# Kernel tuning notes

Hardware: AMD Instinct MI355X
Metric: run time of the kernel (lower is better)

## Reference

```python
import jax, jax.numpy as jnp
import numpy as np

B, L, ENC, DEC, ATT = 64, 1024, 1024, 1024, 1024


def setup_inputs() -> dict:
    key = jax.random.key(0)
    ks = jax.random.split(key, 8)
    s1 = 1.0 / np.sqrt(ENC)
    s2 = 1.0 / np.sqrt(DEC)
    s3 = 1.0 / np.sqrt(ATT)
    return {
        "features": jax.random.normal(ks[0], (B, L, ENC), jnp.float32),
        "hidden_state": jax.random.normal(ks[1], (B, DEC), jnp.float32),
        "W1_w": jax.random.uniform(ks[2], (ENC, ATT), jnp.float32, -s1, s1),
        "W1_b": jax.random.uniform(ks[3], (ATT,), jnp.float32, -s1, s1),
        "W2_w": jax.random.uniform(ks[4], (DEC, ATT), jnp.float32, -s2, s2),
        "W2_b": jax.random.uniform(ks[5], (ATT,), jnp.float32, -s2, s2),
        "V_w": jax.random.uniform(ks[6], (ATT,), jnp.float32, -s3, s3),
        "V_b": jax.random.uniform(ks[7], (), jnp.float32, -s3, s3),
    }


def reference(features, hidden_state, W1_w, W1_b, W2_w, W2_b, V_w, V_b):
    # proj_f: [B, L, ATT]; proj_h: [B, 1, ATT]
    proj_f = jnp.einsum('ble,ea->bla', features, W1_w) + W1_b
    proj_h = (hidden_state @ W2_w + W2_b)[:, None, :]
    scores = jnp.tanh(proj_f + proj_h) @ V_w + V_b  # [B, L]
    alpha = jax.nn.softmax(scores, axis=1)
    context = jnp.einsum('bl,ble->be', alpha, features)
    return alpha, context
```

## Files before the change

### kernel.cpp

```cpp
#include <hip/hip_runtime.h>
#include <hip/hip_bf16.h>


typedef __bf16 bf16x8 __attribute__((ext_vector_type(8)));
typedef float floatx4 __attribute__((ext_vector_type(4)));
typedef unsigned short ushort_t;
typedef unsigned long long u64;

__device__ __forceinline__ ushort_t f2b(float x) {
    union { float f; unsigned u; } v; v.f = x;
    unsigned r = (v.u + 0x7fffu + ((v.u >> 16) & 1u)) >> 16;
    return (ushort_t)r;
}

__device__ __forceinline__ float b2f(ushort_t u) {
    union { unsigned u; float f; } v; v.u = (unsigned)u << 16; return v.f;
}

__device__ __forceinline__ u64 pack4(float4 f) {
    return (u64)f2b(f.x) | ((u64)f2b(f.y) << 16) |
           ((u64)f2b(f.z) << 32) | ((u64)f2b(f.w) << 48);
}

__device__ __forceinline__ void gload_lds16(const void* g, void* l) {
    __builtin_amdgcn_global_load_lds(
        (const __attribute__((address_space(1))) void*)g,
        (__attribute__((address_space(3))) void*)l, 16, 0, 0);
}

__device__ __forceinline__ float fast_tanh(float x) {
    const float ax = fabsf(x);
    const float t  = __expf(-2.0f * ax);
    const float r  = (1.0f - t) * __builtin_amdgcn_rcpf(1.0f + t);
    return copysignf(r, x);
}

__global__ __launch_bounds__(256) void convert_feat_kernel(
    const float* __restrict__ feat, ushort_t* __restrict__ featb) {
    const size_t idx = ((size_t)blockIdx.x * 256 + threadIdx.x) * 8;
    const float4 f0 = *(const float4*)(feat + idx);
    const float4 f1 = *(const float4*)(feat + idx + 4);
    *(u64*)(featb + idx)     = pack4(f0);
    *(u64*)(featb + idx + 4) = pack4(f1);
}

__global__ __launch_bounds__(256) void transpose_w1_kernel(
    const float* __restrict__ w1, ushort_t* __restrict__ w1t) {
    __shared__ ushort_t tile[64][65];
    const int k0 = blockIdx.x * 64, n0 = blockIdx.y * 64;
    const int tr = threadIdx.x >> 6;
    const int tc = threadIdx.x & 63;
#pragma unroll
    for (int i = 0; i < 16; i++) {
        int r = i * 4 + tr;
        tile[tc][r] = f2b(w1[(size_t)(k0 + r) * 1024 + n0 + tc]);
    }
    __syncthreads();
#pragma unroll
    for (int i = 0; i < 16; i++) {
        int r = i * 4 + tr;
        w1t[(size_t)(n0 + r) * 1024 + k0 + tc] = tile[r][tc];
    }
}

__global__ __launch_bounds__(256) void projh_kernel(
    const float* __restrict__ hidden, const float* __restrict__ w2,
    const float* __restrict__ w2b, const float* __restrict__ w1b,
    float* __restrict__ ph) {
    const int b  = blockIdx.y;
    const int al = threadIdx.x & 63;
    const int eg = threadIdx.x >> 6;
    const int a  = blockIdx.x * 64 + al;
    const float* h = hidden + b * 1024;
    float sum = 0.f;
    const int e0 = eg * 256;
#pragma unroll 8
    for (int e = e0; e < e0 + 256; e++)
        sum += h[e] * w2[(size_t)e * 1024 + a];
    __shared__ float red[256];
    red[threadIdx.x] = sum;
    __syncthreads();
    if (threadIdx.x < 64)
        ph[b * 1024 + a] = w2b[a] + w1b[a] + red[al] + red[al + 64] +
                           red[al + 128] + red[al + 192];
}

#define LOG2E2 2.885390082f

__global__ __launch_bounds__(256) void gemm_scores_bf16_kernel(
    const ushort_t* __restrict__ featb,
    const ushort_t* __restrict__ w1t,
    const float* __restrict__ ph,
    const float* __restrict__ vw,
    float* __restrict__ part) {
    __shared__ ushort_t As[128 * 64];
    __shared__ ushort_t Bs[128 * 64];
    __shared__ float cbias[128];
    __shared__ float vvw[128];

    const int tid = threadIdx.x;
    const int lid = blockIdx.y * 8 + blockIdx.x;
    const int c   = lid & 7;
    const int rr  = lid >> 3;
    const int mt  = (rr >> 3) * 8 + c;
    const int nt  = rr & 7;
    const int n0 = nt * 128;
    const int m0 = mt * 128;
    const int b  = m0 >> 10;

    if (tid < 128) {
        cbias[tid] = ph[(b << 10) + n0 + tid];
        vvw[tid]   = vw[n0 + tid];
    }

    const int wave = tid >> 6;
    const int lane = tid & 63;
    const int wr = (wave >> 1) * 64;
    const int wc = (wave & 1) * 64;
    const int q  = lane >> 4;
    const int l15 = lane & 15;

    floatx4 acc[4][4] = {};

    const int srow = lane >> 3;
    const int scol = ((lane & 7) ^ srow) << 3;

    const ushort_t* aBase = featb + (size_t)m0 * 1024;
    const ushort_t* bBase = w1t  + (size_t)n0 * 1024;

    int aoff[4][2], boff[4][2];
#pragma unroll
    for (int t = 0; t < 4; t++) {
        const int ra = wr + t * 16 + l15;
        const int rb = wc + t * 16 + l15;
        aoff[t][0] = ra * 64 + (((q    ) ^ (ra & 7)) << 3);
        aoff[t][1] = ra * 64 + (((q + 4) ^ (ra & 7)) << 3);
        boff[t][0] = rb * 64 + (((q    ) ^ (rb & 7)) << 3);
        boff[t][1] = rb * 64 + (((q + 4) ^ (rb & 7)) << 3);
    }

    for (int kt = 0; kt < 1024; kt += 64) {
#pragma unroll
        for (int p = 0; p < 4; p++) {
            const int seg = wave * 4 + p;
            const int row = seg * 8 + srow;
            gload_lds16(aBase + (size_t)row * 1024 + kt + scol, As + seg * 512);
            gload_lds16(bBase + (size_t)row * 1024 + kt + scol, Bs + seg * 512);
        }
        __syncthreads();
#pragma unroll
        for (int h = 0; h < 2; h++) {
            bf16x8 af[4], bfr[4];
#pragma unroll
            for (int t = 0; t < 4; t++) af[t]  = *(const bf16x8*)&As[aoff[t][h]];
#pragma unroll
            for (int t = 0; t < 4; t++) bfr[t] = *(const bf16x8*)&Bs[boff[t][h]];
#pragma unroll
            for (int tm = 0; tm < 4; tm++)
#pragma unroll
                for (int tn = 0; tn < 4; tn++)
                    acc[tm][tn] = __builtin_amdgcn_mfma_f32_16x16x32_bf16(
                        af[tm], bfr[tn], acc[tm][tn], 0, 0, 0);
        }
        __syncthreads();
    }

    float vv[4], cbk[4];
    float sum_vvw = 0.f;
#pragma unroll
    for (int tn = 0; tn < 4; tn++) {
        const int col = wc + tn * 16 + l15;
        vv[tn]  = vvw[col];
        cbk[tn] = LOG2E2 * cbias[col];
        sum_vvw += vv[tn];
    }
    const int slot = nt * 2 + (wave & 1);
#pragma unroll
    for (int tm = 0; tm < 4; tm++) {
#pragma unroll
        for (int r = 0; r < 4; r++) {
            const int row = wr + tm * 16 + q * 4 + r;
            float s2 = 0.f;
#pragma unroll
            for (int tn = 0; tn < 4; tn++) {
                const float arg = fmaf(LOG2E2, acc[tm][tn][r], cbk[tn]);
                const float e   = __builtin_amdgcn_exp2f(arg);
                s2 = fmaf(__builtin_amdgcn_rcpf(1.0f + e), vv[tn], s2);
            }
            float s = fmaf(-2.0f, s2, sum_vvw);
            s += __shfl_xor(s, 1);
            s += __shfl_xor(s, 2);
            s += __shfl_xor(s, 4);
            s += __shfl_xor(s, 8);
            if (l15 == 0) part[slot * 65536 + m0 + row] = s;
        }
    }
}

__global__ __launch_bounds__(256) void softmax_kernel(
    const float* __restrict__ part, float* __restrict__ alpha) {
    const int b = blockIdx.x;
    const int tid = threadIdx.x;
    __shared__ float red[256];
    float v[4];
    float mx = -1e30f;
#pragma unroll
    for (int i = 0; i < 4; i++) {
        const int m = b * 1024 + tid + i * 256;
        float s = 0.f;
#pragma unroll
        for (int nb = 0; nb < 16; nb++) s += part[nb * 65536 + m];
        v[i] = s;
        mx = fmaxf(mx, s);
    }
    red[tid] = mx; __syncthreads();
    for (int s = 128; s > 0; s >>= 1) {
        if (tid < s) red[tid] = fmaxf(red[tid], red[tid + s]);
        __syncthreads();
    }
    mx = red[0]; __syncthreads();
    float sum = 0.f;
#pragma unroll
    for (int i = 0; i < 4; i++) { v[i] = __expf(v[i] - mx); sum += v[i]; }
    red[tid] = sum; __syncthreads();
    for (int s = 128; s > 0; s >>= 1) {
        if (tid < s) red[tid] += red[tid + s];
        __syncthreads();
    }
    const float inv = 1.0f / red[0];
#pragma unroll
    for (int i = 0; i < 4; i++)
        alpha[b * 1024 + tid + i * 256] = v[i] * inv;
}

__global__ __launch_bounds__(1024) void context_bf16_kernel(
    const float* __restrict__ alpha, const ushort_t* __restrict__ featb,
    float* __restrict__ ctx) {
    const int b  = blockIdx.y;
    const int el = threadIdx.x & 63;
    const int lg = threadIdx.x >> 6;
    const int e  = blockIdx.x * 256 + el * 4;
    const ushort_t* fb = featb + ((size_t)b << 20) + e;
    const float* ab = alpha + b * 1024;
    floatx4 acc = {};
    const int l0 = lg * 64;
#pragma unroll 4
    for (int l = l0; l < l0 + 64; l++) {
        const float a = ab[l];
        const ushort4 u = *(const ushort4*)(fb + (size_t)l * 1024);
        acc[0] = fmaf(a, b2f(u.x), acc[0]);
        acc[1] = fmaf(a, b2f(u.y), acc[1]);
        acc[2] = fmaf(a, b2f(u.z), acc[2]);
        acc[3] = fmaf(a, b2f(u.w), acc[3]);
    }
    __shared__ floatx4 red[16 * 64];
    red[lg * 64 + el] = acc;
    __syncthreads();
#pragma unroll
    for (int s = 8; s > 0; s >>= 1) {
        if (lg < s) red[lg * 64 + el] += red[(lg + s) * 64 + el];
        __syncthreads();
    }
    if (lg == 0)
        *(floatx4*)(ctx + b * 1024 + e) = red[el];
}

__global__ __launch_bounds__(1024) void context_kernel(
    const float* __restrict__ alpha, const float* __restrict__ feat,
    float* __restrict__ ctx) {
    const int b  = blockIdx.y;
    const int el = threadIdx.x & 63;
    const int lg = threadIdx.x >> 6;
    const int e  = blockIdx.x * 256 + el * 4;
    const float* fb = feat + (size_t)b * 1024 * 1024;
    const float* ab = alpha + b * 1024;
    floatx4 acc = {};
    const int l0 = lg * 64;
#pragma unroll 4
    for (int l = l0; l < l0 + 64; l++) {
        const float a = ab[l];
        const floatx4 f = *(const floatx4*)(fb + (size_t)l * 1024 + e);
        acc += a * f;
    }
    __shared__ floatx4 red[16 * 64];
    red[lg * 64 + el] = acc;
    __syncthreads();
#pragma unroll
    for (int s = 8; s > 0; s >>= 1) {
        if (lg < s) red[lg * 64 + el] += red[(lg + s) * 64 + el];
        __syncthreads();
    }
    if (lg == 0)
        *(floatx4*)(ctx + b * 1024 + e) = red[el];
}

#define KP 72
__global__ __launch_bounds__(256) void gemm_scores_f32_kernel(
    const float* __restrict__ feat, const ushort_t* __restrict__ w1t,
    const float* __restrict__ ph, const float* __restrict__ vw,
    float* __restrict__ part) {
    __shared__ ushort_t As[128 * KP];
    __shared__ ushort_t Bs[128 * KP];
    __shared__ float cbias[128];
    __shared__ float vvw[128];
    const int tid = threadIdx.x;
    const int nt = blockIdx.x, n0 = nt * 128, m0 = blockIdx.y * 128;
    const int b = m0 >> 10;
    if (tid < 128) { cbias[tid] = ph[(b << 10) + n0 + tid]; vvw[tid] = vw[n0 + tid]; }
    const int wave = tid >> 6, lane = tid & 63;
    const int wr = (wave >> 1) * 64, wc = (wave & 1) * 64;
    const int q = lane >> 4, l15 = lane & 15;
    floatx4 acc[4][4] = {};
    const int arow = tid >> 4, acol = (tid & 15) * 4;
    const int brow = tid >> 3, bcol = (tid & 7) * 8;
    const float* aptr = feat + (size_t)m0 * 1024;
    const ushort_t* bptr = w1t + (size_t)n0 * 1024;
    for (int kt = 0; kt < 1024; kt += 64) {
#pragma unroll
        for (int p = 0; p < 8; p++) {
            int r = p * 16 + arow;
            const float4 f = *(const float4*)(aptr + (size_t)r * 1024 + kt + acol);
            *(u64*)&As[r * KP + acol] = pack4(f);
        }
#pragma unroll
        for (int p = 0; p < 4; p++) {
            int r = p * 32 + brow;
            *(uint4*)&Bs[r * KP + bcol] =
                *(const uint4*)(bptr + (size_t)r * 1024 + kt + bcol);
        }
        __syncthreads();
#pragma unroll
        for (int ks = 0; ks < 64; ks += 32) {
            bf16x8 af[4], bfr[4];
#pragma unroll
            for (int t = 0; t < 4; t++)
                af[t] = *(const bf16x8*)&As[(wr + t * 16 + l15) * KP + ks + q * 8];
#pragma unroll
            for (int t = 0; t < 4; t++)
                bfr[t] = *(const bf16x8*)&Bs[(wc + t * 16 + l15) * KP + ks + q * 8];
#pragma unroll
            for (int tm = 0; tm < 4; tm++)
#pragma unroll
                for (int tn = 0; tn < 4; tn++)
                    acc[tm][tn] = __builtin_amdgcn_mfma_f32_16x16x32_bf16(
                        af[tm], bfr[tn], acc[tm][tn], 0, 0, 0);
        }
        __syncthreads();
    }
    const int slot = nt * 2 + (wave & 1);
#pragma unroll
    for (int tm = 0; tm < 4; tm++) {
#pragma unroll
        for (int r = 0; r < 4; r++) {
            const int row = wr + tm * 16 + q * 4 + r;
            float s = 0.f;
#pragma unroll
            for (int tn = 0; tn < 4; tn++) {
                const int col = wc + tn * 16 + l15;
                s += fast_tanh(acc[tm][tn][r] + cbias[col]) * vvw[col];
            }
            s += __shfl_xor(s, 1);
            s += __shfl_xor(s, 2);
            s += __shfl_xor(s, 4);
            s += __shfl_xor(s, 8);
            if (l15 == 0) part[slot * 65536 + m0 + row] = s;
        }
    }
}

extern "C" void kernel_launch(void* const* d_in, const int* in_sizes, int n_in,
                              void* d_out, int out_size, void* d_ws, size_t ws_size,
                              hipStream_t stream) {
    const float* feat = (const float*)d_in[0];
    const float* hid  = (const float*)d_in[1];
    const float* w1w  = (const float*)d_in[2];
    const float* w1b  = (const float*)d_in[3];
    const float* w2w  = (const float*)d_in[4];
    const float* w2b  = (const float*)d_in[5];
    const float* vw   = (const float*)d_in[6];

    const size_t FEATB_BYTES = (size_t)64 * 1024 * 1024 * 2;
    const size_t W1T_BYTES   = (size_t)1024 * 1024 * 2;
    const size_t PH_BYTES    = (size_t)64 * 1024 * 4;
    const size_t PART_BYTES  = (size_t)16 * 65536 * 4;
    const bool   big_ws = ws_size >= FEATB_BYTES + W1T_BYTES + PH_BYTES + PART_BYTES;
    if (!big_ws && ws_size < W1T_BYTES + PH_BYTES + PART_BYTES) return;

    char* ws = (char*)d_ws;
    ushort_t* featb = (ushort_t*)ws;
    size_t off = big_ws ? FEATB_BYTES : 0;
    ushort_t* w1t  = (ushort_t*)(ws + off);
    float* ph      = (float*)(ws + off + W1T_BYTES);
    float* part    = (float*)(ws + off + W1T_BYTES + PH_BYTES);

    float* alpha = (float*)d_out;
    float* ctx   = alpha + 64 * 1024;

    transpose_w1_kernel<<<dim3(16, 16), 256, 0, stream>>>(w1w, w1t);
    projh_kernel<<<dim3(16, 64), 256, 0, stream>>>(hid, w2w, w2b, w1b, ph);
    if (big_ws) {
        convert_feat_kernel<<<32768, 256, 0, stream>>>(feat, featb);
        gemm_scores_bf16_kernel<<<dim3(8, 512), 256, 0, stream>>>(
            featb, w1t, ph, vw, part);
        softmax_kernel<<<64, 256, 0, stream>>>(part, alpha);
        context_bf16_kernel<<<dim3(4, 64), 1024, 0, stream>>>(alpha, featb, ctx);
    } else {
        gemm_scores_f32_kernel<<<dim3(8, 512), 256, 0, stream>>>(
            feat, w1t, ph, vw, part);
        softmax_kernel<<<64, 256, 0, stream>>>(part, alpha);
        context_kernel<<<dim3(4, 64), 1024, 0, stream>>>(alpha, feat, ctx);
    }
}
```

Measured before the change: 646.7 us.

## Replace bf16 score GEMM with 256x256 tile double-buffered pipelined kernel

Replaces the 128x128-tile bf16 score GEMM with a 256x256-tile, 512-thread kernel. It double-buffers LDS, splits each K tile into halves and issues global-to-LDS loads for upcoming tiles between MFMA phases, using vmcnt waits and raw barriers. It also raises MFMA priority with s_setprio and remaps workgroup IDs. The aim is to hide load latency, halve operand traffic per flop and cut barrier stalls, at the cost of higher register and LDS use (128 KB LDS) and a more fragile hand-written schedule.

```diff
diff --git a/kernel.cpp b/kernel.cpp
--- a/kernel.cpp
+++ b/kernel.cpp
@@ -34,6 +34,8 @@
     const float r  = (1.0f - t) * __builtin_amdgcn_rcpf(1.0f + t);
     return copysignf(r, x);
 }
+
+#define LOG2E2 2.885390082f
 
 __global__ __launch_bounds__(256) void convert_feat_kernel(
     const float* __restrict__ feat, ushort_t* __restrict__ featb) {
@@ -85,114 +87,138 @@
                            red[al + 128] + red[al + 192];
 }
 
-#define LOG2E2 2.885390082f
-
-__global__ __launch_bounds__(256) void gemm_scores_bf16_kernel(
+
+#define WAITV(n) asm volatile("s_waitcnt vmcnt(" #n ")" ::: "memory")
+#define BAR() __builtin_amdgcn_s_barrier()
+
+#define STG_A(d, h, kc) do { \
+    gload_lds16(aSrc + (kc) + (h) * 32,          aDst + (d) * 16384 + (h) * 8192); \
+    gload_lds16(aSrc + 131072 + (kc) + (h) * 32, aDst + (d) * 16384 + (h) * 8192 + 4096); \
+  } while (0)
+#define STG_B(d, h, kc) do { \
+    gload_lds16(bSrc + (kc) + (h) * 32,          bDst + (d) * 16384 + (h) * 8192); \
+    gload_lds16(bSrc + 131072 + (kc) + (h) * 32, bDst + (d) * 16384 + (h) * 8192 + 4096); \
+  } while (0)
+
+#define PHASE(d, h, mq, LOADB) do { \
+    bf16x8 af[4]; \
+    _Pragma("unroll") \
+    for (int i_ = 0; i_ < 4; i_++) \
+      af[i_] = *(const bf16x8*)(As + (d) * 16384 + (h) * 8192 + \
+                                (ga + (mq) * 4 + i_) * 512 + rdo); \
+    if (LOADB) { \
+      _Pragma("unroll") \
+      for (int j_ = 0; j_ < 4; j_++) \
+        bf[j_] = *(const bf16x8*)(Bs + (d) * 16384 + (h) * 8192 + \
+                                  (gb + j_) * 512 + rdo); \
+    } \
+    __builtin_amdgcn_s_setprio(1); \
+    _Pragma("unroll") \
+    for (int i_ = 0; i_ < 4; i_++) \
+      _Pragma("unroll") \
+      for (int j_ = 0; j_ < 4; j_++) \
+        acc[(mq) * 4 + i_][j_] = __builtin_amdgcn_mfma_f32_16x16x32_bf16( \
+            af[i_], bf[j_], acc[(mq) * 4 + i_][j_], 0, 0, 0); \
+    __builtin_amdgcn_s_setprio(0); \
+  } while (0)
+
+#define TILE(t, d) do { \
+    const int k1_ = (((t) + 1) & 15) * 64; \
+    const int k2_ = (((t) + 2) & 15) * 64; \
+    STG_A(d ^ 1, 1, k1_); \
+    PHASE(d, 0, 0, 1); \
+    STG_B(d ^ 1, 1, k1_); \
+    PHASE(d, 0, 1, 0); \
+    WAITV(8); BAR(); \
+    STG_A(d, 0, k2_); \
+    PHASE(d, 1, 0, 1); \
+    STG_B(d, 0, k2_); \
+    PHASE(d, 1, 1, 0); \
+    WAITV(8); BAR(); \
+  } while (0)
+
+__global__ __launch_bounds__(512, 2) void gemm_scores_256_kernel(
     const ushort_t* __restrict__ featb,
     const ushort_t* __restrict__ w1t,
     const float* __restrict__ ph,
     const float* __restrict__ vw,
     float* __restrict__ part) {
-    __shared__ ushort_t As[128 * 64];
-    __shared__ ushort_t Bs[128 * 64];
-    __shared__ float cbias[128];
-    __shared__ float vvw[128];
+    __shared__ ushort_t As[2 * 16384];
+    __shared__ ushort_t Bs[2 * 16384];
+    __shared__ float cbias[256];
+    __shared__ float vvw[256];
 
     const int tid = threadIdx.x;
-    const int lid = blockIdx.y * 8 + blockIdx.x;
-    const int c   = lid & 7;
-    const int rr  = lid >> 3;
-    const int mt  = (rr >> 3) * 8 + c;
-    const int nt  = rr & 7;
-    const int n0 = nt * 128;
-    const int m0 = mt * 128;
+    const int orig = blockIdx.x;
+    const int wgid = (orig & 7) * 128 + (orig >> 3);
+    const int nt = wgid & 3;
+    const int mt = wgid >> 2;
+    const int n0 = nt * 256;
+    const int m0 = mt * 256;
     const int b  = m0 >> 10;
 
-    if (tid < 128) {
+    if (tid < 256) {
         cbias[tid] = ph[(b << 10) + n0 + tid];
         vvw[tid]   = vw[n0 + tid];
     }
 
-    const int wave = tid >> 6;
+    const int w    = tid >> 6;
     const int lane = tid & 63;
-    const int wr = (wave >> 1) * 64;
-    const int wc = (wave & 1) * 64;
-    const int q  = lane >> 4;
-    const int l15 = lane & 15;
-
-    floatx4 acc[4][4] = {};
-
-    const int srow = lane >> 3;
-    const int scol = ((lane & 7) ^ srow) << 3;
-
-    const ushort_t* aBase = featb + (size_t)m0 * 1024;
-    const ushort_t* bBase = w1t  + (size_t)n0 * 1024;
-
-    int aoff[4][2], boff[4][2];
-#pragma unroll
-    for (int t = 0; t < 4; t++) {
-        const int ra = wr + t * 16 + l15;
-        const int rb = wc + t * 16 + l15;
-        aoff[t][0] = ra * 64 + (((q    ) ^ (ra & 7)) << 3);
-        aoff[t][1] = ra * 64 + (((q + 4) ^ (ra & 7)) << 3);
-        boff[t][0] = rb * 64 + (((q    ) ^ (rb & 7)) << 3);
-        boff[t][1] = rb * 64 + (((q + 4) ^ (rb & 7)) << 3);
-    }
-
-    for (int kt = 0; kt < 1024; kt += 64) {
-#pragma unroll
-        for (int p = 0; p < 4; p++) {
-            const int seg = wave * 4 + p;
-            const int row = seg * 8 + srow;
-            gload_lds16(aBase + (size_t)row * 1024 + kt + scol, As + seg * 512);
-            gload_lds16(bBase + (size_t)row * 1024 + kt + scol, Bs + seg * 512);
-        }
-        __syncthreads();
-#pragma unroll
-        for (int h = 0; h < 2; h++) {
-            bf16x8 af[4], bfr[4];
-#pragma unroll
-            for (int t = 0; t < 4; t++) af[t]  = *(const bf16x8*)&As[aoff[t][h]];
-#pragma unroll
-            for (int t = 0; t < 4; t++) bfr[t] = *(const bf16x8*)&Bs[boff[t][h]];
-#pragma unroll
-            for (int tm = 0; tm < 4; tm++)
-#pragma unroll
-                for (int tn = 0; tn < 4; tn++)
-                    acc[tm][tn] = __builtin_amdgcn_mfma_f32_16x16x32_bf16(
-                        af[tm], bfr[tn], acc[tm][tn], 0, 0, 0);
-        }
-        __syncthreads();
-    }
+    const int q    = lane >> 4;
+    const int l15  = lane & 15;
+    const int rdo  = l15 * 32 + ((q ^ ((l15 >> 1) & 3)) << 3);
+    const int ga   = (w >> 2) * 8;
+    const int gb   = (w & 3) * 4;
+    const int sb   = ((lane & 3) ^ ((lane >> 3) & 3)) << 3;
+
+    const ushort_t* aSrc = featb + (size_t)(m0 + w * 16 + (lane >> 2)) * 1024 + sb;
+    const ushort_t* bSrc = w1t  + (size_t)(n0 + w * 16 + (lane >> 2)) * 1024 + sb;
+    ushort_t* aDst = As + w * 512;
+    ushort_t* bDst = Bs + w * 512;
+
+    floatx4 acc[8][4] = {};
+    bf16x8 bf[4];
+
+    STG_A(0, 0, 0);  STG_B(0, 0, 0);
+    STG_A(0, 1, 0);  STG_B(0, 1, 0);
+    STG_A(1, 0, 64); STG_B(1, 0, 64);
+    WAITV(8); BAR();
+
+    for (int it = 0; it < 8; it++) {
+        TILE(2 * it,     0);
+        TILE(2 * it + 1, 1);
+    }
+    WAITV(0);
 
     float vv[4], cbk[4];
     float sum_vvw = 0.f;
 #pragma unroll
-    for (int tn = 0; tn < 4; tn++) {
-        const int col = wc + tn * 16 + l15;
-        vv[tn]  = vvw[col];
-        cbk[tn] = LOG2E2 * cbias[col];
-        sum_vvw += vv[tn];
-    }
-    const int slot = nt * 2 + (wave & 1);
-#pragma unroll
-    for (int tm = 0; tm < 4; tm++) {
+    for (int j = 0; j < 4; j++) {
+        const int col = (w & 3) * 64 + j * 16 + l15;
+        vv[j]  = vvw[col];
+        cbk[j] = LOG2E2 * cbias[col];
+        sum_vvw += vv[j];
+    }
+    const int slot  = nt * 4 + (w & 3);
+    const int rbase = m0 + (w >> 2) * 128;
+#pragma unroll
+    for (int mf = 0; mf < 8; mf++) {
 #pragma unroll
         for (int r = 0; r < 4; r++) {
-            const int row = wr + tm * 16 + q * 4 + r;
+            const int row = rbase + mf * 16 + q * 4 + r;
             float s2 = 0.f;
 #pragma unroll
-            for (int tn = 0; tn < 4; tn++) {
-                const float arg = fmaf(LOG2E2, acc[tm][tn][r], cbk[tn]);
+            for (int j = 0; j < 4; j++) {
+                const float arg = fmaf(LOG2E2, acc[mf][j][r], cbk[j]);
                 const float e   = __builtin_amdgcn_exp2f(arg);
-                s2 = fmaf(__builtin_amdgcn_rcpf(1.0f + e), vv[tn], s2);
+                s2 = fmaf(__builtin_amdgcn_rcpf(1.0f + e), vv[j], s2);
             }
             float s = fmaf(-2.0f, s2, sum_vvw);
             s += __shfl_xor(s, 1);
             s += __shfl_xor(s, 2);
             s += __shfl_xor(s, 4);
             s += __shfl_xor(s, 8);
-            if (l15 == 0) part[slot * 65536 + m0 + row] = s;
+            if (l15 == 0) part[slot * 65536 + row] = s;
         }
     }
 }
@@ -299,8 +325,8 @@
     const float* __restrict__ feat, const ushort_t* __restrict__ w1t,
     const float* __restrict__ ph, const float* __restrict__ vw,
     float* __restrict__ part) {
-    __shared__ ushort_t As[128 * KP];
-    __shared__ ushort_t Bs[128 * KP];
+    __shared__ ushort_t Asf[128 * KP];
+    __shared__ ushort_t Bsf[128 * KP];
     __shared__ float cbias[128];
     __shared__ float vvw[128];
     const int tid = threadIdx.x;
@@ -320,12 +346,12 @@
         for (int p = 0; p < 8; p++) {
             int r = p * 16 + arow;
             const float4 f = *(const float4*)(aptr + (size_t)r * 1024 + kt + acol);
-            *(u64*)&As[r * KP + acol] = pack4(f);
+            *(u64*)&Asf[r * KP + acol] = pack4(f);
         }
 #pragma unroll
         for (int p = 0; p < 4; p++) {
             int r = p * 32 + brow;
-            *(uint4*)&Bs[r * KP + bcol] =
+            *(uint4*)&Bsf[r * KP + bcol] =
                 *(const uint4*)(bptr + (size_t)r * 1024 + kt + bcol);
         }
         __syncthreads();
@@ -334,10 +360,10 @@
             bf16x8 af[4], bfr[4];
 #pragma unroll
             for (int t = 0; t < 4; t++)
-                af[t] = *(const bf16x8*)&As[(wr + t * 16 + l15) * KP + ks + q * 8];
+                af[t] = *(const bf16x8*)&Asf[(wr + t * 16 + l15) * KP + ks + q * 8];
 #pragma unroll
             for (int t = 0; t < 4; t++)
-                bfr[t] = *(const bf16x8*)&Bs[(wc + t * 16 + l15) * KP + ks + q * 8];
+                bfr[t] = *(const bf16x8*)&Bsf[(wc + t * 16 + l15) * KP + ks + q * 8];
 #pragma unroll
             for (int tm = 0; tm < 4; tm++)
 #pragma unroll
@@ -400,7 +426,7 @@
     projh_kernel<<<dim3(16, 64), 256, 0, stream>>>(hid, w2w, w2b, w1b, ph);
     if (big_ws) {
         convert_feat_kernel<<<32768, 256, 0, stream>>>(feat, featb);
-        gemm_scores_bf16_kernel<<<dim3(8, 512), 256, 0, stream>>>(
+        gemm_scores_256_kernel<<<dim3(1024), 512, 0, stream>>>(
             featb, w1t, ph, vw, part);
         softmax_kernel<<<64, 256, 0, stream>>>(part, alpha);
         context_bf16_kernel<<<dim3(4, 64), 1024, 0, stream>>>(alpha, featb, ctx);
```

Result: faster. 577.4 us (-10.7%).
